# Kernel tuning notes

Hardware: AMD Instinct MI355X
Metric: run time of the kernel (lower is better)

Reference implementation:

```python
import jax, jax.numpy as jnp
import numpy as np

L = 7  # window size (odd)
A = 0.1
B_COEF = 0.9


def mex_hat(d):
    grid = (np.mgrid[:d, :d] - d // 2) * 1.0
    eucl = (grid ** 2).sum(0) ** 0.5
    eucl /= d
    return eucl * np.exp(-eucl)


def setup_inputs() -> dict:
    key = jax.random.key(0)
    x = jax.random.normal(key, (16, 1, 512, 512), dtype=jnp.float32)
    kernel = jnp.asarray(mex_hat(L).reshape(-1), dtype=jnp.float32)  # [49], row-major like unfold
    return {"x": x, "kernel": kernel}


def reference(x, kernel):
    # x: [B,1,H,W], kernel: [L*L]
    # Extract zero-padded LxL patches, matching F.unfold(padding=L//2) ordering
    # (C=1, kernel positions row-major). patches: [B, L*L, H, W]
    patches = jax.lax.conv_general_dilated_patches(
        x, (L, L), (1, 1), 'SAME')
    average_term = jnp.exp(-patches.mean(axis=1, keepdims=True))  # [B,1,H,W]
    differential_term = jnp.sum(
        kernel[None, :, None, None] * jax.nn.relu(patches - x),
        axis=1, keepdims=True)  # [B,1,H,W]
    suppression = A * average_term + B_COEF * differential_term
    norm = jnp.sqrt(jnp.sum(suppression ** 2))
    suppression = suppression / norm
    mask = jnp.where(x > suppression, jnp.ones_like(x), jnp.zeros_like(x))
    return mask, average_term, differential_term
```

## Files before the change

kernel.cpp:

```cpp
#include <hip/hip_runtime.h>
#include <math.h>

#define HW 512
#define NB 16
#define TX 16
#define TY 16
#define LDSW 24
#define LDSH 22
#define N_PIX (NB * HW * HW)
#define NBLK (32 * 32 * NB)

using f32x4 = __attribute__((ext_vector_type(4))) float;

__device__ __forceinline__ float sgpr_f(float v) {
    return __uint_as_float(__builtin_amdgcn_readfirstlane(__float_as_uint(v)));
}

__global__ __launch_bounds__(64, 6) void li_phase1(
    const float* __restrict__ x, const float* __restrict__ kw,
    float* __restrict__ out_ratio, float* __restrict__ out_avg,
    float* __restrict__ out_dif, float* __restrict__ partials)
{
    __shared__ float tile[LDSH * LDSW];

    const int tid = threadIdx.x;
    const int bx = blockIdx.x, by = blockIdx.y, b = blockIdx.z;
    const int x0 = bx * TX, y0 = by * TY;
    const float* xb = x + (size_t)b * (HW * HW);

    float w[49];
    float W = 0.f;
#pragma unroll
    for (int i = 0; i < 49; i++) { w[i] = sgpr_f(kw[i]); W += w[i]; }

#pragma unroll
    for (int k = 0; k < 3; k++) {
        const int idx = tid + k * 64;
        if (idx < LDSH * (LDSW / 4)) {
            const int r  = idx / (LDSW / 4);
            const int c4 = idx - r * (LDSW / 4);
            const int gy = y0 - 3 + r;
            const int gx = x0 - 4 + c4 * 4;
            float4 v = make_float4(0.f, 0.f, 0.f, 0.f);
            if ((unsigned)gy < HW && (unsigned)gx <= (unsigned)(HW - 4))
                v = *(const float4*)(xb + gy * HW + gx);
            *(float4*)&tile[r * LDSW + c4 * 4] = v;
        }
    }
    __syncthreads();

    const int cx = tid & 3;
    const int cy = tid >> 2;
    const int colw = 4 * cx;

    float cen[4];
    {
        float4 c4v = *(const float4*)&tile[(cy + 3) * LDSW + colw + 4];
        cen[0] = c4v.x; cen[1] = c4v.y; cen[2] = c4v.z; cen[3] = c4v.w;
    }

    float dif[4]  = {0.f, 0.f, 0.f, 0.f};
    float bsum[4] = {0.f, 0.f, 0.f, 0.f};

#pragma unroll
    for (int di = 0; di < 7; di++) {
        const float* base = &tile[(cy + di) * LDSW + colw];
        float4 q0 = *(const float4*)base;
        float4 q1 = *(const float4*)(base + 4);
        float4 q2 = *(const float4*)(base + 8);
        float v[12] = {q0.x, q0.y, q0.z, q0.w,
                       q1.x, q1.y, q1.z, q1.w,
                       q2.x, q2.y, q2.z, q2.w};

        float s0 = ((v[1] + v[2]) + (v[3] + v[4])) + ((v[5] + v[6]) + v[7]);
        float s1 = s0 + (v[8]  - v[1]);
        float s2 = s1 + (v[9]  - v[2]);
        float s3 = s2 + (v[10] - v[3]);
        bsum[0] += s0; bsum[1] += s1; bsum[2] += s2; bsum[3] += s3;

#pragma unroll
        for (int dj = 0; dj < 7; dj++) {
            if (di == 3 && dj == 3) continue;
            const float wv = w[di * 7 + dj];
#pragma unroll
            for (int j = 0; j < 4; j++)
                dif[j] = fmaf(wv, fmaxf(v[1 + j + dj], cen[j]), dif[j]);
        }
    }

    const size_t gi = (size_t)b * (HW * HW) + (size_t)(y0 + cy) * HW + x0 + colw;
    float av[4], dv[4], rv[4];
    float ss = 0.f;
#pragma unroll
    for (int j = 0; j < 4; j++) {
        av[j] = __expf(-bsum[j] * (1.0f / 49.0f));
        dv[j] = fmaf(-W, cen[j], dif[j]);
        const float spv = 0.1f * av[j] + 0.9f * dv[j];
        rv[j] = cen[j] * __builtin_amdgcn_rcpf(spv);
        ss = fmaf(spv, spv, ss);
    }
    *(f32x4*)(out_avg + gi)   = (f32x4){av[0], av[1], av[2], av[3]};
    *(f32x4*)(out_dif + gi)   = (f32x4){dv[0], dv[1], dv[2], dv[3]};
    *(f32x4*)(out_ratio + gi) = (f32x4){rv[0], rv[1], rv[2], rv[3]};

#pragma unroll
    for (int off = 32; off > 0; off >>= 1)
        ss += __shfl_down(ss, off, 64);
    if (tid == 0)
        partials[bx + 32 * (by + 32 * b)] = ss;
}

__global__ __launch_bounds__(256) void li_phase2(
    const float* __restrict__ partials, float* __restrict__ io)
{
    __shared__ float wsum[4];
    __shared__ float s_inv;
    const int tid = threadIdx.x;

    float s = 0.f;
#pragma unroll
    for (int i = 0; i < NBLK / 256; i++)
        s += partials[tid + i * 256];
#pragma unroll
    for (int off = 32; off > 0; off >>= 1)
        s += __shfl_down(s, off, 64);
    if ((tid & 63) == 0) wsum[tid >> 6] = s;
    __syncthreads();
    if (tid == 0)
        s_inv = 1.0f / sqrtf((wsum[0] + wsum[1]) + (wsum[2] + wsum[3]));
    __syncthreads();

    const float inv = s_inv;
    const int base = blockIdx.x * 4096 + tid * 4;
#pragma unroll
    for (int k = 0; k < 4; k++) {
        const int i = base + k * 1024;
        float4 r = *(const float4*)(io + i);
        float4 m;
        m.x = (r.x > inv) ? 1.f : 0.f;
        m.y = (r.y > inv) ? 1.f : 0.f;
        m.z = (r.z > inv) ? 1.f : 0.f;
        m.w = (r.w > inv) ? 1.f : 0.f;
        *(float4*)(io + i) = m;
    }
}

extern "C" void kernel_launch(void* const* d_in, const int* in_sizes, int n_in,
                              void* d_out, int out_size, void* d_ws, size_t ws_size,
                              hipStream_t stream) {
    const float* x  = (const float*)d_in[0];
    const float* kw = (const float*)d_in[1];
    float* out   = (float*)d_out;
    float* ratio = out;
    float* avg   = out + N_PIX;
    float* dif   = out + 2 * (size_t)N_PIX;
    float* ws    = (float*)d_ws;

    dim3 g(HW / TX, HW / TY, NB);
    li_phase1<<<g, 64, 0, stream>>>(x, kw, ratio, avg, dif, ws);
    li_phase2<<<N_PIX / 4096, 256, 0, stream>>>(ws, ratio);
}
```

Baseline: 111.5 us.

## Use 32x8 per-wave tiles in 256-thread blocks without barriers

Each block now holds four independent wavefronts, each with its own LDS slice covering a 32x8 output tile. The block-wide barrier is dropped because every wave reads only its own slice. Wider rows are meant to improve global load coalescing, and larger blocks cut block scheduling overhead. The halo overhead per tile changes slightly, and the partial-sum indexing is adapted to the new tile count.

```diff
diff --git a/kernel.cpp b/kernel.cpp
--- a/kernel.cpp
+++ b/kernel.cpp
@@ -3,12 +3,14 @@
 
 #define HW 512
 #define NB 16
-#define TX 16
-#define TY 16
-#define LDSW 24
-#define LDSH 22
+#define WTX 32
+#define WTY 8
+#define LDSW 40
+#define LDSH 14
+#define SLICE (LDSH * LDSW)
 #define N_PIX (NB * HW * HW)
-#define NBLK (32 * 32 * NB)
+#define NTILE (16 * 64 * NB)
+#define NBLK (NTILE / 4)
 
 using f32x4 = __attribute__((ext_vector_type(4))) float;
 
@@ -16,17 +18,21 @@
     return __uint_as_float(__builtin_amdgcn_readfirstlane(__float_as_uint(v)));
 }
 
-__global__ __launch_bounds__(64, 6) void li_phase1(
+__global__ __launch_bounds__(256, 8) void li_phase1(
     const float* __restrict__ x, const float* __restrict__ kw,
     float* __restrict__ out_ratio, float* __restrict__ out_avg,
     float* __restrict__ out_dif, float* __restrict__ partials)
 {
-    __shared__ float tile[LDSH * LDSW];
+    __shared__ float tile4[4 * SLICE];
 
-    const int tid = threadIdx.x;
-    const int bx = blockIdx.x, by = blockIdx.y, b = blockIdx.z;
-    const int x0 = bx * TX, y0 = by * TY;
+    const int tid  = threadIdx.x;
+    const int w4   = tid >> 6;
+    const int lane = tid & 63;
+    const int bx = blockIdx.x, byg = blockIdx.y, b = blockIdx.z;
+    const int x0 = bx * WTX;
+    const int y0 = byg * 32 + w4 * WTY;
     const float* xb = x + (size_t)b * (HW * HW);
+    float* tile = &tile4[w4 * SLICE];
 
     float w[49];
     float W = 0.f;
@@ -35,7 +41,7 @@
 
 #pragma unroll
     for (int k = 0; k < 3; k++) {
-        const int idx = tid + k * 64;
+        const int idx = lane + k * 64;
         if (idx < LDSH * (LDSW / 4)) {
             const int r  = idx / (LDSW / 4);
             const int c4 = idx - r * (LDSW / 4);
@@ -47,15 +53,14 @@
             *(float4*)&tile[r * LDSW + c4 * 4] = v;
         }
     }
-    __syncthreads();
 
-    const int cx = tid & 3;
-    const int cy = tid >> 2;
-    const int colw = 4 * cx;
+    const int lx = lane & 7;
+    const int ly = lane >> 3;
+    const int colw = 4 * lx;
 
     float cen[4];
     {
-        float4 c4v = *(const float4*)&tile[(cy + 3) * LDSW + colw + 4];
+        float4 c4v = *(const float4*)&tile[(ly + 3) * LDSW + colw + 4];
         cen[0] = c4v.x; cen[1] = c4v.y; cen[2] = c4v.z; cen[3] = c4v.w;
     }
 
@@ -64,7 +69,7 @@
 
 #pragma unroll
     for (int di = 0; di < 7; di++) {
-        const float* base = &tile[(cy + di) * LDSW + colw];
+        const float* base = &tile[(ly + di) * LDSW + colw];
         float4 q0 = *(const float4*)base;
         float4 q1 = *(const float4*)(base + 4);
         float4 q2 = *(const float4*)(base + 8);
@@ -88,7 +93,7 @@
         }
     }
 
-    const size_t gi = (size_t)b * (HW * HW) + (size_t)(y0 + cy) * HW + x0 + colw;
+    const size_t gi = (size_t)b * (HW * HW) + (size_t)(y0 + ly) * HW + x0 + colw;
     float av[4], dv[4], rv[4];
     float ss = 0.f;
 #pragma unroll
@@ -106,8 +111,8 @@
 #pragma unroll
     for (int off = 32; off > 0; off >>= 1)
         ss += __shfl_down(ss, off, 64);
-    if (tid == 0)
-        partials[bx + 32 * (by + 32 * b)] = ss;
+    if (lane == 0)
+        partials[bx + 16 * ((byg * 4 + w4) + 64 * b)] = ss;
 }
 
 __global__ __launch_bounds__(256) void li_phase2(
@@ -119,7 +124,7 @@
 
     float s = 0.f;
 #pragma unroll
-    for (int i = 0; i < NBLK / 256; i++)
+    for (int i = 0; i < NTILE / 256; i++)
         s += partials[tid + i * 256];
 #pragma unroll
     for (int off = 32; off > 0; off >>= 1)
@@ -156,7 +161,7 @@
     float* dif   = out + 2 * (size_t)N_PIX;
     float* ws    = (float*)d_ws;
 
-    dim3 g(HW / TX, HW / TY, NB);
-    li_phase1<<<g, 64, 0, stream>>>(x, kw, ratio, avg, dif, ws);
+    dim3 g(HW / WTX, HW / 32, NB);
+    li_phase1<<<g, 256, 0, stream>>>(x, kw, ratio, avg, dif, ws);
     li_phase2<<<N_PIX / 4096, 256, 0, stream>>>(ws, ratio);
 }
```

New measurement: 143.1 us. 28.4% more time.
